# Kernel optimization log

Measured on AMD Instinct MI355X. Metric: run time of the kernel, lower is better.

Reference implementation:

```python
import jax, jax.numpy as jnp
import numpy as np

EPS = 1.1920929e-07  # torch.finfo(float32).eps (nn.RMSNorm default eps=None)
ROPE_BASE = 10000.0


def _rmsnorm(x, g):
    # x: (..., d). torch nn.RMSNorm: x * rsqrt(mean(x^2) + eps) * g
    var = jnp.mean(jnp.square(x), axis=-1, keepdims=True)
    return x * jax.lax.rsqrt(var + EPS) * g


def _rope(x):
    # x: (b, h, s, d). Matches RotaryPositionEmbedding: half-split concat layout.
    s, d = x.shape[2], x.shape[3]
    pos = jnp.arange(s, dtype=x.dtype)[:, None]                      # (s,1)
    freqs = ROPE_BASE ** (-jnp.arange(0, d, 2, dtype=x.dtype) / d)   # (d/2,)
    ang = pos * freqs                                                # (s, d/2)
    c, sn = jnp.cos(ang), jnp.sin(ang)
    xe, xo = x[..., ::2], x[..., 1::2]
    return jnp.concatenate([xe * c - xo * sn, xe * sn + xo * c], axis=-1)


def setup_inputs() -> dict:
    key = jax.random.key(0)
    ks = jax.random.split(key, 9)
    B, S, D, F = 1, 2048, 4096, 11008
    W = 0.02  # weight scale to keep activations sane
    return {
        "x": jax.random.normal(ks[0], (B, S, D), jnp.float32),
        "wq": jax.random.normal(ks[1], (D, D), jnp.float32) * W,
        "wk": jax.random.normal(ks[2], (D, D), jnp.float32) * W,
        "wv": jax.random.normal(ks[3], (D, D), jnp.float32) * W,
        "wo": jax.random.normal(ks[4], (D, D), jnp.float32) * W,
        "w1": jax.random.normal(ks[5], (D, F), jnp.float32) * W,
        "w2": jax.random.normal(ks[6], (F, D), jnp.float32) * W,
        "w3": jax.random.normal(ks[7], (D, F), jnp.float32) * W,
        "g_attn": jnp.ones((D,), jnp.float32),
        "g_ffn": jnp.ones((D,), jnp.float32),
    }


def reference(x, wq, wk, wv, wo, w1, w2, w3, g_attn, g_ffn):
    n_heads = 32
    bsz, seqlen, dim = x.shape
    head_dim = dim // n_heads

    h = _rmsnorm(x, g_attn)
    # (b,s,d) @ (d,d) -> (b,s,h,hd) -> (b,h,s,hd)
    xq = (h @ wq).reshape(bsz, seqlen, n_heads, head_dim).transpose(0, 2, 1, 3)
    xk = (h @ wk).reshape(bsz, seqlen, n_heads, head_dim).transpose(0, 2, 1, 3)
    xv = (h @ wv).reshape(bsz, seqlen, n_heads, head_dim).transpose(0, 2, 1, 3)

    xq = _rope(xq)
    xk = _rope(xk)

    # NOTE: faithful to source: NO 1/sqrt(head_dim) scaling, NO causal mask.
    scores = jnp.einsum("bhqd,bhkd->bhqk", xq, xk)
    scores = jax.nn.softmax(scores, axis=-1)
    out = jnp.einsum("bhqk,bhkd->bhqd", scores, xv)        # (b,h,s,hd)
    out = out.transpose(0, 2, 1, 3).reshape(bsz, seqlen, dim)
    xo = out @ wo

    # NOTE: faithful to source: no residual connections; silu on w3 branch.
    h2 = _rmsnorm(xo, g_ffn)
    x1 = h2 @ w1
    x3 = jax.nn.silu(h2 @ w3)
    return (x1 * x3) @ w2
```

## Files before the change

### kernel.cpp

```cpp
#include <hip/hip_runtime.h>
#include <math.h>

typedef unsigned short u16;
typedef short short8 __attribute__((ext_vector_type(8)));
typedef _Float16 half8 __attribute__((ext_vector_type(8)));
typedef float f32x4 __attribute__((ext_vector_type(4)));

#define DEV static __device__ __forceinline__

DEV float bf2f(u16 h) { union { unsigned int u; float f; } v; v.u = ((unsigned int)h) << 16; return v.f; }
DEV u16 f2bf(float f) {
  union { float f; unsigned int u; } v; v.f = f;
  unsigned int r = v.u + 0x7FFFu + ((v.u >> 16) & 1u);
  return (u16)(r >> 16);
}
DEV u16 f2h(float f) { union { _Float16 h; u16 u; } v; v.h = (_Float16)f; return v.u; }
DEV float h2f(u16 b) { union { u16 u; _Float16 h; } v; v.u = b; return (float)v.h; }

DEV void gl_lds16(const void* g, void* l) {
  __builtin_amdgcn_global_load_lds(
      (const __attribute__((address_space(1))) unsigned int*)g,
      (__attribute__((address_space(3))) unsigned int*)l, 16, 0, 0);
}

template <int N> DEV void vm_wait() {
  if constexpr (N == 0) asm volatile("s_waitcnt vmcnt(0)" ::: "memory");
  else if constexpr (N == 6) asm volatile("s_waitcnt vmcnt(6)" ::: "memory");
  else if constexpr (N == 8) asm volatile("s_waitcnt vmcnt(8)" ::: "memory");
  else static_assert(N == 0 || N == 6 || N == 8, "add literal");
}

DEV void lgkm0_pin() {
  asm volatile("s_waitcnt lgkmcnt(0)" ::: "memory");
  __builtin_amdgcn_sched_barrier(0);
}

DEV void xcd_swizzle(int& bx, int& by) {
  int gx = gridDim.x, gy = gridDim.y;
  int lin = by * gx + bx;
  int xcd = lin & 7, i = lin >> 3;
  if ((gx & 7) == 0) {
    int cx = gx >> 3;
    bx = xcd * cx + i % cx;
    by = i / cx;
  } else {
    int cpx = (gx * gy) >> 3;
    int swz = xcd * cpx + i;
    bx = swz % gx;
    by = swz / gx;
  }
}

template <bool SPLIT>
__global__ __launch_bounds__(256) void rmsnorm_kernel(
    const float* __restrict__ x, const float* __restrict__ g,
    u16* __restrict__ oh, u16* __restrict__ ol) {
  int row = blockIdx.x, t = threadIdx.x;
  const float* xr = x + (size_t)row * 4096;
  float4 vals[4];
  float s = 0.f;
#pragma unroll
  for (int i = 0; i < 4; i++) {
    vals[i] = ((const float4*)xr)[t + i * 256];
    s += vals[i].x * vals[i].x + vals[i].y * vals[i].y + vals[i].z * vals[i].z + vals[i].w * vals[i].w;
  }
#pragma unroll
  for (int m = 1; m < 64; m <<= 1) s += __shfl_xor(s, m);
  __shared__ float red[4];
  if ((t & 63) == 0) red[t >> 6] = s;
  __syncthreads();
  s = red[0] + red[1] + red[2] + red[3];
  float rinv = rsqrtf(s * (1.f / 4096.f) + 1.1920929e-07f);
#pragma unroll
  for (int i = 0; i < 4; i++) {
    float4 gv = ((const float4*)g)[t + i * 256];
    float4 v = vals[i];
    float f[4] = {v.x * rinv * gv.x, v.y * rinv * gv.y, v.z * rinv * gv.z, v.w * rinv * gv.w};
    ushort4 rh, rl;
    u16* hp = (u16*)&rh; u16* lp = (u16*)&rl;
#pragma unroll
    for (int j = 0; j < 4; j++) {
      u16 hi = f2bf(f[j]);
      hp[j] = hi;
      if (SPLIT) lp[j] = f2bf(f[j] - bf2f(hi));
    }
    ((ushort4*)(oh + (size_t)row * 4096))[t + i * 256] = rh;
    if (SPLIT) ((ushort4*)(ol + (size_t)row * 4096))[t + i * 256] = rl;
  }
}

__global__ void tconv_kernel(const float* __restrict__ in, u16* __restrict__ out, int K, int N) {
  __shared__ float tile[64][65];
  int k0 = blockIdx.y * 64, n0 = blockIdx.x * 64;
  int tx = threadIdx.x, ty = threadIdx.y;
#pragma unroll
  for (int i = 0; i < 8; i++) {
    int r = ty + 8 * i;
    float2 v = *(const float2*)&in[(size_t)(k0 + r) * N + n0 + tx * 2];
    tile[r][tx * 2] = v.x;
    tile[r][tx * 2 + 1] = v.y;
  }
  __syncthreads();
#pragma unroll
  for (int i = 0; i < 8; i++) {
    int c = ty + 8 * i;
    ushort2 o;
    o.x = f2bf(tile[tx * 2][c]);
    o.y = f2bf(tile[tx * 2 + 1][c]);
    *(ushort2*)&out[(size_t)(n0 + c) * K + k0 + tx * 2] = o;
  }
}

__global__ void tconv_ilv_kernel(const float* __restrict__ in, u16* __restrict__ out,
                                 int K, int N, int off) {
  __shared__ float tile[64][65];
  int k0 = blockIdx.y * 64, n0 = blockIdx.x * 64;
  int tx = threadIdx.x, ty = threadIdx.y;
#pragma unroll
  for (int i = 0; i < 8; i++) {
    int r = ty + 8 * i;
    float2 v = *(const float2*)&in[(size_t)(k0 + r) * N + n0 + tx * 2];
    tile[r][tx * 2] = v.x;
    tile[r][tx * 2 + 1] = v.y;
  }
  __syncthreads();
#pragma unroll
  for (int i = 0; i < 8; i++) {
    int c = ty + 8 * i;
    int n = n0 + c;
    int orow = ((n >> 7) << 8) + (n & 127) + off;
    ushort2 o;
    o.x = f2bf(tile[tx * 2][c]);
    o.y = f2bf(tile[tx * 2 + 1][c]);
    *(ushort2*)&out[(size_t)orow * K + k0 + tx * 2] = o;
  }
}

__global__ void tconv_split_kernel(const float* __restrict__ in, u16* __restrict__ oh,
                                   u16* __restrict__ ol, int K, int N) {
  __shared__ float tile[64][65];
  int k0 = blockIdx.y * 64, n0 = blockIdx.x * 64;
  int tx = threadIdx.x, ty = threadIdx.y;
#pragma unroll
  for (int i = 0; i < 8; i++) {
    int r = ty + 8 * i;
    float2 v = *(const float2*)&in[(size_t)(k0 + r) * N + n0 + tx * 2];
    tile[r][tx * 2] = v.x;
    tile[r][tx * 2 + 1] = v.y;
  }
  __syncthreads();
#pragma unroll
  for (int i = 0; i < 8; i++) {
    int c = ty + 8 * i;
    float f0 = tile[tx * 2][c], f1 = tile[tx * 2 + 1][c];
    u16 h0 = f2bf(f0), h1 = f2bf(f1);
    ushort2 vh, vl;
    vh.x = h0; vh.y = h1;
    vl.x = f2bf(f0 - bf2f(h0)); vl.y = f2bf(f1 - bf2f(h1));
    size_t idx = (size_t)(n0 + c) * K + k0 + tx * 2;
    *(ushort2*)&oh[idx] = vh;
    *(ushort2*)&ol[idx] = vl;
  }
}

__global__ __launch_bounds__(256) void rope_table_kernel(float* __restrict__ tab) {
  int i = blockIdx.x * 256 + threadIdx.x;
  int j = i & 63, s = i >> 6;
  double freq = pow(10000.0, -(double)j / 64.0);
  double ang = (double)s * freq;
  tab[i * 2] = (float)cos(ang);
  tab[i * 2 + 1] = (float)sin(ang);
}

__global__ __launch_bounds__(256) void rope_inplace_kernel(
    u16* q, const float* __restrict__ tab) {
  int idx = blockIdx.x * 256 + threadIdx.x;
  int j = idx & 63, hd = (idx >> 6) & 63, s = idx >> 12;
  size_t base = (size_t)s * 8192 + hd * 128;
  float xe = h2f(q[base + 2 * j]);
  float xo = h2f(q[base + 2 * j + 1]);
  float cs = tab[(s * 64 + j) * 2], sn = tab[(s * 64 + j) * 2 + 1];
  q[base + j] = f2h(xe * cs - xo * sn);
  q[base + 64 + j] = f2h(xe * sn + xo * cs);
}

template <int OUT, bool TRIK>
__global__ __launch_bounds__(512, 2) void gemm8_kernel(
    const u16* __restrict__ A, const u16* __restrict__ A2,
    const u16* __restrict__ B, const u16* __restrict__ B2,
    void* __restrict__ C, u16* __restrict__ C2,
    int M, int N, int K, int lda, int ldb) {
  __shared__ __attribute__((aligned(16))) u16 SMEM[65536];
  int t = threadIdx.x, l = t & 63, w = t >> 6;
  int bx = blockIdx.x, by = blockIdx.y;
  xcd_swizzle(bx, by);
  int m0 = by * 256, n0 = bx * 256;
  int wm = w >> 2, wn = w & 3, bh = wn >> 1;
  f32x4 acc[8][4] = {};
  int nk = K >> 6;

  auto AsP = [&](int d, int h) -> u16* { return SMEM + (d * 2 + h) * 8192; };
  auto BsP = [&](int d, int h) -> u16* { return SMEM + 32768 + (d * 2 + h) * 8192; };

  auto stageA = [&](int kt, int dd) {
    const u16* Ab = A; int kc = kt << 6;
    if (TRIK) { int seg = kt >> 6; Ab = (seg == 1) ? A2 : A; kc = (kt & 63) << 6; }
#pragma unroll
    for (int i = 0; i < 4; i++) {
      int id = i * 512 + t;
      int hh = id >> 10, idc = id & 1023;
      int r = idc >> 3, cb = idc & 7;
      int csw = ((cb * 16) ^ ((r & 7) << 4)) >> 1;
      gl_lds16(&Ab[(size_t)(m0 + hh * 128 + r) * lda + kc + csw], AsP(dd, hh) + idc * 8);
    }
  };
  auto stageB = [&](int kt, int dd) {
    const u16* Bb = B; int kc = kt << 6;
    if (TRIK) { int seg = kt >> 6; Bb = (seg == 2) ? B2 : B; kc = (kt & 63) << 6; }
#pragma unroll
    for (int i = 0; i < 4; i++) {
      int id = i * 512 + t;
      int hh = id >> 10, idc = id & 1023;
      int r = idc >> 3, cb = idc & 7;
      int csw = ((cb * 16) ^ ((r & 7) << 4)) >> 1;
      gl_lds16(&Bb[(size_t)(n0 + hh * 128 + r) * ldb + kc + csw], BsP(dd, hh) + idc * 8);
    }
  };

  int lq = l >> 4, lr = l & 15;
  short8 af[4][2], bf[4][2];
  auto rdA = [&](int d, int mh) {
    const char* Ax = (const char*)AsP(d, wm);
#pragma unroll
    for (int m = 0; m < 4; m++) {
      int r = mh * 64 + m * 16 + lr;
      int rb = r * 128, rx = (r & 7) << 4;
#pragma unroll
      for (int kh = 0; kh < 2; kh++)
        af[m][kh] = *(const short8*)(Ax + rb + ((kh * 64 + lq * 16) ^ rx));
    }
  };
  auto rdB2 = [&](int d, int nlo, int nhi) {
    const char* Bx = (const char*)BsP(d, bh);
#pragma unroll
    for (int n = 0; n < 4; n++) {
      if (n < nlo || n >= nhi) continue;
      int r = (wn & 1) * 64 + n * 16 + lr;
      int rb = r * 128, rx = (r & 7) << 4;
#pragma unroll
      for (int kh = 0; kh < 2; kh++)
        bf[n][kh] = *(const short8*)(Bx + rb + ((kh * 64 + lq * 16) ^ rx));
    }
  };
  auto mm8 = [&](int mo, int no) {
    __builtin_amdgcn_s_setprio(1);
#pragma unroll
    for (int m = 0; m < 4; m++)
#pragma unroll
      for (int n = 0; n < 2; n++)
#pragma unroll
        for (int kh = 0; kh < 2; kh++)
          acc[mo + m][no + n] =
              __builtin_amdgcn_mfma_f32_16x16x32_bf16(af[m][kh], bf[no + n][kh], acc[mo + m][no + n], 0, 0, 0);
    __builtin_amdgcn_s_setprio(0);
  };

  stageB(0, 0); stageA(0, 0);
  stageB(1, 1); stageA(1, 1);
  vm_wait<8>();
  __builtin_amdgcn_s_barrier();

  for (int kt = 0; kt < nk; ++kt) {
    int d = kt & 1;
    rdA(d, 0);
    rdB2(d, 0, 2);
    __builtin_amdgcn_s_barrier();
    lgkm0_pin();
    mm8(0, 0);
    __builtin_amdgcn_s_barrier();
    rdB2(d, 2, 4);
    __builtin_amdgcn_s_barrier();
    lgkm0_pin();
    mm8(0, 2);
    __builtin_amdgcn_s_barrier();
    rdA(d, 1);
    if (kt + 2 < nk) stageB(kt + 2, d);
    __builtin_amdgcn_s_barrier();
    lgkm0_pin();
    mm8(4, 2);
    __builtin_amdgcn_s_barrier();
    if (kt + 2 < nk) stageA(kt + 2, d);
    __builtin_amdgcn_s_barrier();
    mm8(4, 0);
    if (kt + 2 < nk) vm_wait<8>();
    else vm_wait<0>();
    __builtin_amdgcn_s_barrier();
  }

  if (OUT == 3) {
    __syncthreads();
    float* EPI = (float*)SMEM;
    if (wn >= 2) {
#pragma unroll
      for (int m = 0; m < 8; m++)
#pragma unroll
        for (int i = 0; i < 4; i++) {
          int rl = wm * 128 + m * 16 + lq * 4 + i;
#pragma unroll
          for (int n = 0; n < 4; n++)
            EPI[rl * 128 + (wn - 2) * 64 + n * 16 + lr] = acc[m][n][i];
        }
    }
    __syncthreads();
    if (wn < 2) {
      u16* Ob = (u16*)C;
      int cb = n0 >> 1;
#pragma unroll
      for (int m = 0; m < 8; m++)
#pragma unroll
        for (int i = 0; i < 4; i++) {
          int rl = wm * 128 + m * 16 + lq * 4 + i;
          int row = m0 + rl;
#pragma unroll
          for (int n = 0; n < 4; n++) {
            float a = acc[m][n][i];
            float b = EPI[rl * 128 + wn * 64 + n * 16 + lr];
            float r = a * (b / (1.f + expf(-b)));
            Ob[(size_t)row * N + cb + wn * 64 + n * 16 + lr] = f2bf(r);
          }
        }
    }
    return;
  }

#pragma unroll
  for (int m = 0; m < 8; m++) {
#pragma unroll
    for (int i = 0; i < 4; i++) {
      int row = m0 + wm * 128 + m * 16 + lq * 4 + i;
      size_t rb = (size_t)row * N + n0 + wn * 64 + lr;
#pragma unroll
      for (int n = 0; n < 4; n++) {
        float f = acc[m][n][i];
        if (OUT == 0) ((float*)C)[rb + n * 16] = f;
        else if (OUT == 1) ((u16*)C)[rb + n * 16] = f2bf(f);
        else if (OUT == 4) ((u16*)C)[rb + n * 16] = f2h(f);
        else {
          u16 hi = f2bf(f);
          ((u16*)C)[rb + n * 16] = hi;
          C2[rb + n * 16] = f2bf(f - bf2f(hi));
        }
      }
    }
  }
}

template <int OUT>
__global__ __launch_bounds__(512, 2) void gemm8n_kernel(
    const u16* __restrict__ A, const u16* __restrict__ B, void* __restrict__ C,
    int M, int N, int K, int lda, int ldb) {
  __shared__ __attribute__((aligned(16))) u16 As[2][128 * 64];
  __shared__ __attribute__((aligned(16))) u16 Bs3[3][256 * 64];
  int t = threadIdx.x, l = t & 63, w = t >> 6;
  int bx = blockIdx.x, by = blockIdx.y;
  xcd_swizzle(bx, by);
  int m0 = by * 128, n0 = bx * 256;
  int wm = w >> 2, wn = w & 3;
  f32x4 acc[4][4] = {};
  int nk = K >> 6;

  auto stageA = [&](int kt, int dd) {
    int kc = kt << 6;
#pragma unroll
    for (int i = 0; i < 2; i++) {
      int id = i * 512 + t;
      int r = id >> 3, cb = id & 7;
      int csw = ((cb * 16) ^ ((r & 7) << 4)) >> 1;
      gl_lds16(&A[(size_t)(m0 + r) * lda + kc + csw], &As[dd][id * 8]);
    }
  };
  auto stageB = [&](int kt, int bb) {
    int kc = kt << 6;
#pragma unroll
    for (int i = 0; i < 4; i++) {
      int id = i * 512 + t;
      int r = id >> 3, cb = id & 7;
      int csw = ((cb * 16) ^ ((r & 7) << 4)) >> 1;
      gl_lds16(&B[(size_t)(n0 + r) * ldb + kc + csw], &Bs3[bb][id * 8]);
    }
  };

  int lq = l >> 4, lr = l & 15;
  short8 af0[4], af1[4], bf0[4], bf1[4];
  auto rdA4 = [&](short8 (&dst)[4], int d, int kh) {
    const char* Ax = (const char*)As[d];
#pragma unroll
    for (int m = 0; m < 4; m++) {
      int r = wm * 64 + m * 16 + lr;
      dst[m] = *(const short8*)(Ax + r * 128 + ((kh * 64 + lq * 16) ^ ((r & 7) << 4)));
    }
  };
  auto rdB4 = [&](short8 (&dst)[4], int bb, int kh) {
    const char* Bx = (const char*)Bs3[bb];
#pragma unroll
    for (int n = 0; n < 4; n++) {
      int r = wn * 64 + n * 16 + lr;
      dst[n] = *(const short8*)(Bx + r * 128 + ((kh * 64 + lq * 16) ^ ((r & 7) << 4)));
    }
  };
  auto mm16 = [&](short8 (&a)[4], short8 (&b)[4]) {
    __builtin_amdgcn_s_setprio(1);
#pragma unroll
    for (int m = 0; m < 4; m++)
#pragma unroll
      for (int n = 0; n < 4; n++)
        acc[m][n] = __builtin_amdgcn_mfma_f32_16x16x32_bf16(a[m], b[n], acc[m][n], 0, 0, 0);
    __builtin_amdgcn_s_setprio(0);
  };

  stageB(0, 0); stageA(0, 0);
  stageB(1, 1); stageA(1, 1);
  vm_wait<6>();
  __builtin_amdgcn_s_barrier();

  for (int kt = 0; kt < nk; ++kt) {
    int d = kt & 1;
    int bb = kt % 3, bb2 = (kt + 2) % 3;
    if (kt + 2 < nk) stageB(kt + 2, bb2);
    rdA4(af0, d, 0); rdB4(bf0, bb, 0);
    __builtin_amdgcn_s_barrier();
    lgkm0_pin();
    mm16(af0, bf0);
    __builtin_amdgcn_s_barrier();
    rdA4(af1, d, 1); rdB4(bf1, bb, 1);
    lgkm0_pin();
    __builtin_amdgcn_s_barrier();
    if (kt + 2 < nk) { stageA(kt + 2, d); vm_wait<6>(); }
    else vm_wait<0>();
    mm16(af1, bf1);
    __builtin_amdgcn_s_barrier();
  }
  if (OUT == 2) {
    u16* Cb = (u16*)C;
#pragma unroll
    for (int m = 0; m < 4; m++) {
      int sbase = m0 + wm * 64 + m * 16 + lq * 4;
#pragma unroll
      for (int n = 0; n < 4; n++) {
        int dg = n0 + wn * 64 + n * 16 + lr;
        ushort4 pk;
        pk.x = f2bf(acc[m][n][0]); pk.y = f2bf(acc[m][n][1]);
        pk.z = f2bf(acc[m][n][2]); pk.w = f2bf(acc[m][n][3]);
        *(ushort4*)&Cb[(size_t)dg * M + sbase] = pk;
      }
    }
    return;
  }
#pragma unroll
  for (int m = 0; m < 4; m++) {
#pragma unroll
    for (int i = 0; i < 4; i++) {
      int row = m0 + wm * 64 + m * 16 + lq * 4 + i;
      size_t rb = (size_t)row * N + n0 + wn * 64 + lr;
#pragma unroll
      for (int n = 0; n < 4; n++) {
        float f = acc[m][n][i];
        if (OUT == 0) ((float*)C)[rb + n * 16] = f;
        else ((u16*)C)[rb + n * 16] = f2bf(f);
      }
    }
  }
}

__global__ __launch_bounds__(256, 2) void attn_kernel(
    const u16* __restrict__ qf16, const u16* __restrict__ kf16,
    const u16* __restrict__ vt, u16* __restrict__ out) {
  const int QS = 8192;
  __shared__ __attribute__((aligned(16))) u16 KH[64 * 128];
  __shared__ __attribute__((aligned(16))) u16 Vl[128 * 64];
  __shared__ __attribute__((aligned(16))) u16 Pl[8][16 * 72];
  int t = threadIdx.x, l = t & 63, w = t >> 6;
  int hd = blockIdx.y, q0 = blockIdx.x * 128;
  int lr = l & 15, lq = l >> 4;
  int qrow0 = q0 + (w * 2) * 16 + lr;
  int qrow1 = q0 + (w * 2 + 1) * 16 + lr;
  half8 qf[2][4];
#pragma unroll
  for (int g = 0; g < 2; g++) {
    size_t qoff = (size_t)(g ? qrow1 : qrow0) * QS + hd * 128 + lq * 8;
#pragma unroll
    for (int kc = 0; kc < 4; kc++)
      qf[g][kc] = *(const half8*)&qf16[qoff + kc * 32];
  }
  f32x4 accO[2][8] = {};
  float mrun[2] = {-__builtin_inff(), -__builtin_inff()};
  float lrun[2] = {0.f, 0.f};
  for (int kv0 = 0; kv0 < 2048; kv0 += 64) {
#pragma unroll
    for (int i = 0; i < 4; i++) {
      int ci = i * 256 + t;
      int row = ci >> 4;
      int cb = (ci & 15) ^ (row & 7);
      gl_lds16(&kf16[(size_t)(kv0 + row) * QS + hd * 128 + cb * 8], &KH[ci * 8]);
    }
#pragma unroll
    for (int i = 0; i < 4; i++) {
      int ci = i * 256 + t;
      int row = ci >> 3;
      int cb = (ci & 7) ^ (row & 7);
      gl_lds16(&vt[((size_t)hd * 128 + row) * 2048 + kv0 + cb * 8], &Vl[ci * 8]);
    }
    __syncthreads();
#pragma unroll
    for (int g = 0; g < 2; g++) {
      f32x4 accS[4];
#pragma unroll
      for (int mm = 0; mm < 4; mm++) {
        accS[mm] = (f32x4){0.f, 0.f, 0.f, 0.f};
#pragma unroll
        for (int kc = 0; kc < 4; kc++) {
          int rowk = mm * 16 + lr;
          int phys = (rowk * 256 + kc * 64 + lq * 16) ^ ((rowk & 7) << 4);
          half8 a_h = *(const half8*)((const char*)KH + phys);
          accS[mm] = __builtin_amdgcn_mfma_f32_16x16x32_f16(a_h, qf[g][kc], accS[mm], 0, 0, 0);
        }
      }
      float tmax = -__builtin_inff();
#pragma unroll
      for (int mm = 0; mm < 4; mm++)
        tmax = fmaxf(tmax, fmaxf(fmaxf(accS[mm][0], accS[mm][1]), fmaxf(accS[mm][2], accS[mm][3])));
      tmax = fmaxf(tmax, __shfl_xor(tmax, 16));
      tmax = fmaxf(tmax, __shfl_xor(tmax, 32));
      float mnew = fmaxf(mrun[g], tmax);
      float scale = expf(mrun[g] - mnew);
      float psum = 0.f;
      u16* Pw = &Pl[w * 2 + g][0];
#pragma unroll
      for (int mm = 0; mm < 4; mm++) {
        float p0 = expf(accS[mm][0] - mnew), p1 = expf(accS[mm][1] - mnew);
        float p2 = expf(accS[mm][2] - mnew), p3 = expf(accS[mm][3] - mnew);
        psum += (p0 + p1) + (p2 + p3);
        ushort4 pk;
        pk.x = f2bf(p0); pk.y = f2bf(p1); pk.z = f2bf(p2); pk.w = f2bf(p3);
        *(ushort4*)&Pw[lr * 72 + mm * 16 + lq * 4] = pk;
      }
      psum += __shfl_xor(psum, 16);
      psum += __shfl_xor(psum, 32);
      lrun[g] = lrun[g] * scale + psum;
      mrun[g] = mnew;
#pragma unroll
      for (int mm = 0; mm < 8; mm++) accO[g][mm] = accO[g][mm] * scale;
#pragma unroll
      for (int kc2 = 0; kc2 < 2; kc2++) {
        short8 bp = *(const short8*)((const char*)Pw + lr * 144 + kc2 * 64 + lq * 16);
#pragma unroll
        for (int mm = 0; mm < 8; mm++) {
          int rowd = mm * 16 + lr;
          int phys = (rowd * 128 + kc2 * 64 + lq * 16) ^ ((rowd & 7) << 4);
          short8 av = *(const short8*)((const char*)Vl + phys);
          accO[g][mm] = __builtin_amdgcn_mfma_f32_16x16x32_bf16(av, bp, accO[g][mm], 0, 0, 0);
        }
      }
    }
    __syncthreads();
  }
#pragma unroll
  for (int g = 0; g < 2; g++) {
    float rinv = 1.f / lrun[g];
    int qrow = g ? qrow1 : qrow0;
#pragma unroll
    for (int mm = 0; mm < 8; mm++) {
      ushort4 pk;
      pk.x = f2bf(accO[g][mm][0] * rinv); pk.y = f2bf(accO[g][mm][1] * rinv);
      pk.z = f2bf(accO[g][mm][2] * rinv); pk.w = f2bf(accO[g][mm][3] * rinv);
      *(ushort4*)&out[(size_t)qrow * 4096 + hd * 128 + mm * 16 + lq * 4] = pk;
    }
  }
}

extern "C" void kernel_launch(void* const* d_in, const int* in_sizes, int n_in,
                              void* d_out, int out_size, void* d_ws, size_t ws_size,
                              hipStream_t stream) {
  const float* x      = (const float*)d_in[0];
  const float* wq     = (const float*)d_in[1];
  const float* wk     = (const float*)d_in[2];
  const float* wv     = (const float*)d_in[3];
  const float* wo     = (const float*)d_in[4];
  const float* w1     = (const float*)d_in[5];
  const float* w2     = (const float*)d_in[6];
  const float* w3     = (const float*)d_in[7];
  const float* g_attn = (const float*)d_in[8];
  const float* g_ffn  = (const float*)d_in[9];

  char* ws = (char*)d_ws;
  char* R0 = ws;
  char* R1 = R0 + (size_t)22016 * 4096 * 2;
  char* R2 = R1 + (size_t)8192 * 4096 * 2;
  char* R3 = R2 + (size_t)2 * 2048 * 4096 * 2;
  char* R4 = R3 + (size_t)2048 * 8192 * 2;
  char* RT = R4 + (size_t)2 * 2048 * 4096 * 2;
  (void)ws_size; (void)in_sizes; (void)n_in; (void)out_size;

  u16* wA     = (u16*)R0;
  u16* wB     = (u16*)R1;
  u16* h_hi   = (u16*)R2;
  u16* h_lo   = (u16*)(R2 + (size_t)2048 * 4096 * 2);
  u16* qk     = (u16*)R3;
  u16* ao     = (u16*)R4;
  u16* vT     = (u16*)(R4 + (size_t)2048 * 4096 * 2);
  float* xo   = (float*)R1;
  u16* h2     = (u16*)(R1 + (size_t)2048 * 4096 * 4);
  u16* x1silu = (u16*)R3;
  float* tab  = (float*)RT;
  x1silu = (u16*)R2;

  dim3 tb(32, 8);

  rope_table_kernel<<<512, 256, 0, stream>>>(tab);
  rmsnorm_kernel<true><<<2048, 256, 0, stream>>>(x, g_attn, h_hi, h_lo);
  tconv_split_kernel<<<dim3(64, 64), tb, 0, stream>>>(wq, wA, wB, 4096, 4096);
  tconv_split_kernel<<<dim3(64, 64), tb, 0, stream>>>(wk, wA + (size_t)4096 * 4096, wB + (size_t)4096 * 4096, 4096, 4096);
  gemm8_kernel<4, true><<<dim3(32, 8), 512, 0, stream>>>(
      h_hi, h_lo, wA, wB, qk, nullptr, 2048, 8192, 12288, 4096, 4096);
  rope_inplace_kernel<<<32768, 256, 0, stream>>>(qk, tab);
  tconv_kernel<<<dim3(64, 64), tb, 0, stream>>>(wv, wA, 4096, 4096);
  gemm8n_kernel<2><<<dim3(16, 16), 512, 0, stream>>>(h_hi, wA, vT, 2048, 4096, 4096, 4096, 4096);
  attn_kernel<<<dim3(16, 32), 256, 0, stream>>>(qk, qk + 4096, vT, ao);
  tconv_kernel<<<dim3(64, 64), tb, 0, stream>>>(wo, wA, 4096, 4096);
  gemm8n_kernel<0><<<dim3(16, 16), 512, 0, stream>>>(ao, wA, xo, 2048, 4096, 4096, 4096, 4096);
  rmsnorm_kernel<false><<<2048, 256, 0, stream>>>(xo, g_ffn, h2, nullptr);
  tconv_ilv_kernel<<<dim3(172, 64), tb, 0, stream>>>(w1, wA, 4096, 11008, 0);
  tconv_ilv_kernel<<<dim3(172, 64), tb, 0, stream>>>(w3, wA, 4096, 11008, 128);
  gemm8_kernel<3, false><<<dim3(86, 8), 512, 0, stream>>>(
      h2, nullptr, wA, nullptr, x1silu, nullptr, 2048, 11008, 4096, 4096, 4096);
  tconv_kernel<<<dim3(64, 172), tb, 0, stream>>>(w2, wA, 11008, 4096);
  gemm8n_kernel<0><<<dim3(16, 16), 512, 0, stream>>>(x1silu, wA, (float*)d_out, 2048, 4096, 11008, 11008, 11008);
}
```

Measured before the change: 1.627 ms.

## Switch QK/V projections and attention PV to fp16, drop third split term

Changes the Q/K/V projection path from a three-term bf16 split (hi*hi, lo*hi, hi*lo) to fp16 with a two-term split on the activations only. This cuts the QK GEMM's K dimension from 12288 to 8192 and removes the low-part weight conversion kernels. It also makes the V projection and the attention PV product use fp16 MFMA. The aim is less MFMA work and less weight conversion traffic while keeping accuracy through fp16's extra mantissa bits, at the cost of fp16 range and overflow risk.

Measured after the change: 1.468 ms. 1.11x faster.

```diff
diff --git a/kernel.cpp b/kernel.cpp
--- a/kernel.cpp
+++ b/kernel.cpp
@@ -33,6 +33,14 @@
 DEV void lgkm0_pin() {
   asm volatile("s_waitcnt lgkmcnt(0)" ::: "memory");
   __builtin_amdgcn_sched_barrier(0);
+}
+
+template <int DT>
+DEV f32x4 mm_frag(short8 a, short8 b, f32x4 c) {
+  if constexpr (DT == 0)
+    return __builtin_amdgcn_mfma_f32_16x16x32_bf16(a, b, c, 0, 0, 0);
+  else
+    return __builtin_amdgcn_mfma_f32_16x16x32_f16(*(half8*)&a, *(half8*)&b, c, 0, 0, 0);
 }
 
 DEV void xcd_swizzle(int& bx, int& by) {
@@ -80,15 +88,20 @@
     u16* hp = (u16*)&rh; u16* lp = (u16*)&rl;
 #pragma unroll
     for (int j = 0; j < 4; j++) {
-      u16 hi = f2bf(f[j]);
-      hp[j] = hi;
-      if (SPLIT) lp[j] = f2bf(f[j] - bf2f(hi));
+      if (SPLIT) {
+        u16 hi = f2h(f[j]);
+        hp[j] = hi;
+        lp[j] = f2h(f[j] - h2f(hi));
+      } else {
+        hp[j] = f2bf(f[j]);
+      }
     }
     ((ushort4*)(oh + (size_t)row * 4096))[t + i * 256] = rh;
     if (SPLIT) ((ushort4*)(ol + (size_t)row * 4096))[t + i * 256] = rl;
   }
 }
 
+template <bool F16>
 __global__ void tconv_kernel(const float* __restrict__ in, u16* __restrict__ out, int K, int N) {
   __shared__ float tile[64][65];
   int k0 = blockIdx.y * 64, n0 = blockIdx.x * 64;
@@ -105,8 +118,8 @@
   for (int i = 0; i < 8; i++) {
     int c = ty + 8 * i;
     ushort2 o;
-    o.x = f2bf(tile[tx * 2][c]);
-    o.y = f2bf(tile[tx * 2 + 1][c]);
+    o.x = F16 ? f2h(tile[tx * 2][c]) : f2bf(tile[tx * 2][c]);
+    o.y = F16 ? f2h(tile[tx * 2 + 1][c]) : f2bf(tile[tx * 2 + 1][c]);
     *(ushort2*)&out[(size_t)(n0 + c) * K + k0 + tx * 2] = o;
   }
 }
@@ -133,33 +146,6 @@
     o.x = f2bf(tile[tx * 2][c]);
     o.y = f2bf(tile[tx * 2 + 1][c]);
     *(ushort2*)&out[(size_t)orow * K + k0 + tx * 2] = o;
-  }
-}
-
-__global__ void tconv_split_kernel(const float* __restrict__ in, u16* __restrict__ oh,
-                                   u16* __restrict__ ol, int K, int N) {
-  __shared__ float tile[64][65];
-  int k0 = blockIdx.y * 64, n0 = blockIdx.x * 64;
-  int tx = threadIdx.x, ty = threadIdx.y;
-#pragma unroll
-  for (int i = 0; i < 8; i++) {
-    int r = ty + 8 * i;
-    float2 v = *(const float2*)&in[(size_t)(k0 + r) * N + n0 + tx * 2];
-    tile[r][tx * 2] = v.x;
-    tile[r][tx * 2 + 1] = v.y;
-  }
-  __syncthreads();
-#pragma unroll
-  for (int i = 0; i < 8; i++) {
-    int c = ty + 8 * i;
-    float f0 = tile[tx * 2][c], f1 = tile[tx * 2 + 1][c];
-    u16 h0 = f2bf(f0), h1 = f2bf(f1);
-    ushort2 vh, vl;
-    vh.x = h0; vh.y = h1;
-    vl.x = f2bf(f0 - bf2f(h0)); vl.y = f2bf(f1 - bf2f(h1));
-    size_t idx = (size_t)(n0 + c) * K + k0 + tx * 2;
-    *(ushort2*)&oh[idx] = vh;
-    *(ushort2*)&ol[idx] = vl;
   }
 }
 
@@ -184,11 +170,11 @@
   q[base + 64 + j] = f2h(xe * sn + xo * cs);
 }
 
-template <int OUT, bool TRIK>
+template <int OUT, bool TRIK, int DT>
 __global__ __launch_bounds__(512, 2) void gemm8_kernel(
     const u16* __restrict__ A, const u16* __restrict__ A2,
-    const u16* __restrict__ B, const u16* __restrict__ B2,
-    void* __restrict__ C, u16* __restrict__ C2,
+    const u16* __restrict__ B,
+    void* __restrict__ C,
     int M, int N, int K, int lda, int ldb) {
   __shared__ __attribute__((aligned(16))) u16 SMEM[65536];
   int t = threadIdx.x, l = t & 63, w = t >> 6;
@@ -215,15 +201,15 @@
     }
   };
   auto stageB = [&](int kt, int dd) {
-    const u16* Bb = B; int kc = kt << 6;
-    if (TRIK) { int seg = kt >> 6; Bb = (seg == 2) ? B2 : B; kc = (kt & 63) << 6; }
+    int kc = kt << 6;
+    if (TRIK) kc = (kt & 63) << 6;
 #pragma unroll
     for (int i = 0; i < 4; i++) {
       int id = i * 512 + t;
       int hh = id >> 10, idc = id & 1023;
       int r = idc >> 3, cb = idc & 7;
       int csw = ((cb * 16) ^ ((r & 7) << 4)) >> 1;
-      gl_lds16(&Bb[(size_t)(n0 + hh * 128 + r) * ldb + kc + csw], BsP(dd, hh) + idc * 8);
+      gl_lds16(&B[(size_t)(n0 + hh * 128 + r) * ldb + kc + csw], BsP(dd, hh) + idc * 8);
     }
   };
 
@@ -260,8 +246,7 @@
       for (int n = 0; n < 2; n++)
 #pragma unroll
         for (int kh = 0; kh < 2; kh++)
-          acc[mo + m][no + n] =
-              __builtin_amdgcn_mfma_f32_16x16x32_bf16(af[m][kh], bf[no + n][kh], acc[mo + m][no + n], 0, 0, 0);
+          acc[mo + m][no + n] = mm_frag<DT>(af[m][kh], bf[no + n][kh], acc[mo + m][no + n]);
     __builtin_amdgcn_s_setprio(0);
   };
 
@@ -344,18 +329,13 @@
         float f = acc[m][n][i];
         if (OUT == 0) ((float*)C)[rb + n * 16] = f;
         else if (OUT == 1) ((u16*)C)[rb + n * 16] = f2bf(f);
-        else if (OUT == 4) ((u16*)C)[rb + n * 16] = f2h(f);
-        else {
-          u16 hi = f2bf(f);
-          ((u16*)C)[rb + n * 16] = hi;
-          C2[rb + n * 16] = f2bf(f - bf2f(hi));
-        }
+        else ((u16*)C)[rb + n * 16] = f2h(f);
       }
     }
   }
 }
 
-template <int OUT>
+template <int OUT, int DT>
 __global__ __launch_bounds__(512, 2) void gemm8n_kernel(
     const u16* __restrict__ A, const u16* __restrict__ B, void* __restrict__ C,
     int M, int N, int K, int lda, int ldb) {
@@ -414,7 +394,7 @@
     for (int m = 0; m < 4; m++)
 #pragma unroll
       for (int n = 0; n < 4; n++)
-        acc[m][n] = __builtin_amdgcn_mfma_f32_16x16x32_bf16(a[m], b[n], acc[m][n], 0, 0, 0);
+        acc[m][n] = mm_frag<DT>(a[m], b[n], acc[m][n]);
     __builtin_amdgcn_s_setprio(0);
   };
 
@@ -449,8 +429,13 @@
       for (int n = 0; n < 4; n++) {
         int dg = n0 + wn * 64 + n * 16 + lr;
         ushort4 pk;
-        pk.x = f2bf(acc[m][n][0]); pk.y = f2bf(acc[m][n][1]);
-        pk.z = f2bf(acc[m][n][2]); pk.w = f2bf(acc[m][n][3]);
+        if (DT == 1) {
+          pk.x = f2h(acc[m][n][0]); pk.y = f2h(acc[m][n][1]);
+          pk.z = f2h(acc[m][n][2]); pk.w = f2h(acc[m][n][3]);
+        } else {
+          pk.x = f2bf(acc[m][n][0]); pk.y = f2bf(acc[m][n][1]);
+          pk.z = f2bf(acc[m][n][2]); pk.w = f2bf(acc[m][n][3]);
+        }
         *(ushort4*)&Cb[(size_t)dg * M + sbase] = pk;
       }
     }
@@ -541,7 +526,7 @@
         float p2 = expf(accS[mm][2] - mnew), p3 = expf(accS[mm][3] - mnew);
         psum += (p0 + p1) + (p2 + p3);
         ushort4 pk;
-        pk.x = f2bf(p0); pk.y = f2bf(p1); pk.z = f2bf(p2); pk.w = f2bf(p3);
+        pk.x = f2h(p0); pk.y = f2h(p1); pk.z = f2h(p2); pk.w = f2h(p3);
         *(ushort4*)&Pw[lr * 72 + mm * 16 + lq * 4] = pk;
       }
       psum += __shfl_xor(psum, 16);
@@ -552,13 +537,13 @@
       for (int mm = 0; mm < 8; mm++) accO[g][mm] = accO[g][mm] * scale;
 #pragma unroll
       for (int kc2 = 0; kc2 < 2; kc2++) {
-        short8 bp = *(const short8*)((const char*)Pw + lr * 144 + kc2 * 64 + lq * 16);
+        half8 bp = *(const half8*)((const char*)Pw + lr * 144 + kc2 * 64 + lq * 16);
 #pragma unroll
         for (int mm = 0; mm < 8; mm++) {
           int rowd = mm * 16 + lr;
           int phys = (rowd * 128 + kc2 * 64 + lq * 16) ^ ((rowd & 7) << 4);
-          short8 av = *(const short8*)((const char*)Vl + phys);
-          accO[g][mm] = __builtin_amdgcn_mfma_f32_16x16x32_bf16(av, bp, accO[g][mm], 0, 0, 0);
+          half8 av = *(const half8*)((const char*)Vl + phys);
+          accO[g][mm] = __builtin_amdgcn_mfma_f32_16x16x32_f16(av, bp, accO[g][mm], 0, 0, 0);
         }
       }
     }
@@ -602,7 +587,6 @@
   (void)ws_size; (void)in_sizes; (void)n_in; (void)out_size;
 
   u16* wA     = (u16*)R0;
-  u16* wB     = (u16*)R1;
   u16* h_hi   = (u16*)R2;
   u16* h_lo   = (u16*)(R2 + (size_t)2048 * 4096 * 2);
   u16* qk     = (u16*)R3;
@@ -610,29 +594,28 @@
   u16* vT     = (u16*)(R4 + (size_t)2048 * 4096 * 2);
   float* xo   = (float*)R1;
   u16* h2     = (u16*)(R1 + (size_t)2048 * 4096 * 4);
-  u16* x1silu = (u16*)R3;
+  u16* x1silu = (u16*)R2;
   float* tab  = (float*)RT;
-  x1silu = (u16*)R2;
 
   dim3 tb(32, 8);
 
   rope_table_kernel<<<512, 256, 0, stream>>>(tab);
   rmsnorm_kernel<true><<<2048, 256, 0, stream>>>(x, g_attn, h_hi, h_lo);
-  tconv_split_kernel<<<dim3(64, 64), tb, 0, stream>>>(wq, wA, wB, 4096, 4096);
-  tconv_split_kernel<<<dim3(64, 64), tb, 0, stream>>>(wk, wA + (size_t)4096 * 4096, wB + (size_t)4096 * 4096, 4096, 4096);
-  gemm8_kernel<4, true><<<dim3(32, 8), 512, 0, stream>>>(
-      h_hi, h_lo, wA, wB, qk, nullptr, 2048, 8192, 12288, 4096, 4096);
+  tconv_kernel<true><<<dim3(64, 64), tb, 0, stream>>>(wq, wA, 4096, 4096);
+  tconv_kernel<true><<<dim3(64, 64), tb, 0, stream>>>(wk, wA + (size_t)4096 * 4096, 4096, 4096);
+  gemm8_kernel<4, true, 1><<<dim3(32, 8), 512, 0, stream>>>(
+      h_hi, h_lo, wA, qk, 2048, 8192, 8192, 4096, 4096);
   rope_inplace_kernel<<<32768, 256, 0, stream>>>(qk, tab);
-  tconv_kernel<<<dim3(64, 64), tb, 0, stream>>>(wv, wA, 4096, 4096);
-  gemm8n_kernel<2><<<dim3(16, 16), 512, 0, stream>>>(h_hi, wA, vT, 2048, 4096, 4096, 4096, 4096);
+  tconv_kernel<true><<<dim3(64, 64), tb, 0, stream>>>(wv, wA, 4096, 4096);
+  gemm8n_kernel<2, 1><<<dim3(16, 16), 512, 0, stream>>>(h_hi, wA, vT, 2048, 4096, 4096, 4096, 4096);
   attn_kernel<<<dim3(16, 32), 256, 0, stream>>>(qk, qk + 4096, vT, ao);
-  tconv_kernel<<<dim3(64, 64), tb, 0, stream>>>(wo, wA, 4096, 4096);
-  gemm8n_kernel<0><<<dim3(16, 16), 512, 0, stream>>>(ao, wA, xo, 2048, 4096, 4096, 4096, 4096);
+  tconv_kernel<false><<<dim3(64, 64), tb, 0, stream>>>(wo, wA, 4096, 4096);
+  gemm8n_kernel<0, 0><<<dim3(16, 16), 512, 0, stream>>>(ao, wA, xo, 2048, 4096, 4096, 4096, 4096);
   rmsnorm_kernel<false><<<2048, 256, 0, stream>>>(xo, g_ffn, h2, nullptr);
   tconv_ilv_kernel<<<dim3(172, 64), tb, 0, stream>>>(w1, wA, 4096, 11008, 0);
   tconv_ilv_kernel<<<dim3(172, 64), tb, 0, stream>>>(w3, wA, 4096, 11008, 128);
-  gemm8_kernel<3, false><<<dim3(86, 8), 512, 0, stream>>>(
-      h2, nullptr, wA, nullptr, x1silu, nullptr, 2048, 11008, 4096, 4096, 4096);
-  tconv_kernel<<<dim3(64, 172), tb, 0, stream>>>(w2, wA, 11008, 4096);
-  gemm8n_kernel<0><<<dim3(16, 16), 512, 0, stream>>>(x1silu, wA, (float*)d_out, 2048, 4096, 11008, 11008, 11008);
-}
+  gemm8_kernel<3, false, 0><<<dim3(86, 8), 512, 0, stream>>>(
+      h2, nullptr, wA, x1silu, 2048, 11008, 4096, 4096, 4096);
+  tconv_kernel<false><<<dim3(64, 172), tb, 0, stream>>>(w2, wA, 11008, 4096);
+  gemm8n_kernel<0, 0><<<dim3(16, 16), 512, 0, stream>>>(x1silu, wA, (float*)d_out, 2048, 4096, 11008, 11008, 11008);
+}
```
